# Kernel optimization log

Measured on AMD Instinct MI355X. Metric: run time of the kernel, lower is better.

Reference implementation:

```python
import jax, jax.numpy as jnp
import numpy as np

B, N, H = 8, 128, 512   # batch, num_sent (n == m required by the 'all' branch), hidden_size
D = 2 * H               # bi-LSTM output dim
SCALE = 0.05


def setup_inputs() -> dict:
    key = jax.random.key(0)
    ks = jax.random.split(key, 24)
    p = lambda k, shape: (jax.random.normal(k, shape, dtype=jnp.float32) * SCALE)
    return {
        "x0_enc": jax.random.normal(ks[0], (B, N, D), dtype=jnp.float32),
        "x1_enc": jax.random.normal(ks[1], (B, N, D), dtype=jnp.float32),
        # concat_attention
        "Wc1": p(ks[2], (D, H)), "Wc2": p(ks[3], (D, H)), "vc": p(ks[4], (H,)),
        # bilinear_attention
        "Wb": p(ks[5], (D, D)),
        # dot_attention x2 (separate params)
        "Wd1": p(ks[6], (D, H)), "vd1": p(ks[7], (H,)),
        "Wd2": p(ks[8], (D, H)), "vd2": p(ks[9], (H,)),
        # minus_attention (Ws/vs are unused in forward)
        "Wm": p(ks[10], (D, H)), "vm": p(ks[11], (H,)),
        # aggregation_layer
        "Wq": p(ks[12], (D, H)), "vq": p(ks[13], (H,)),
        "Wp1": p(ks[14], (2 * D, H)), "Wp2": p(ks[15], (D, H)), "vp": p(ks[16], (H,)),
        "Wpred": p(ks[17], (2 * D, 2)), "bpred": jnp.zeros((2,), dtype=jnp.float32),
    }


def _dot_att(x, y, Wd, vd):
    # sjt[b,m,n] = vd . tanh(Wd(x[b,n] * y[b,m]))  -- pairwise elementwise product + MLP
    z = jnp.tanh(jnp.einsum("bnd,bmd,dh->bmnh", x, y, Wd))  # [B,m,n,H]
    s = jnp.einsum("bmnh,h->bmn", z, vd)
    a = jax.nn.softmax(s, axis=2)
    return jnp.einsum("bmn,bnd->bmd", a, x)


def _minus_att(x, y, Wm, vm):
    # Wm is linear, so Wm(x_n - y_m) = (x@Wm)_n - (y@Wm)_m
    a, b = x @ Wm, y @ Wm                                    # [B,n,H], [B,m,H]
    z = jnp.tanh(a[:, None, :, :] - b[:, :, None, :])        # [B,m,n,H]
    s = jnp.einsum("bmnh,h->bmn", z, vm)
    att = jax.nn.softmax(s, axis=2)
    return jnp.einsum("bmn,bnd->bmd", att, x)


def _concat_att(x, y, Wc1, Wc2, vc):
    a, b = x @ Wc1, y @ Wc2                                  # [B,n,H], [B,m,H]
    z = jnp.tanh(a[:, None, :, :] + b[:, :, None, :])        # [B,m,n,H]
    s = jnp.einsum("bmnh,h->bmn", z, vc)
    att = jax.nn.softmax(s, axis=2)
    return jnp.einsum("bmn,bnd->bmd", att, x)


def _bilinear_att(x, y, Wb):
    s = jnp.einsum("bmd,bnd->bmn", y, x @ Wb)
    att = jax.nn.softmax(s, axis=2)
    return jnp.einsum("bmn,bnd->bmd", att, x)


def reference(x0_enc, x1_enc, Wc1, Wc2, vc, Wb, Wd1, vd1, Wd2, vd2, Wm, vm,
              Wq, vq, Wp1, Wp2, vp, Wpred, bpred):
    x0, x1 = x0_enc, x1_enc
    # attention_fx('all')
    qtc = _concat_att(x0, x1, Wc1, Wc2, vc)
    qtb = _bilinear_att(x0, x1, Wb)
    qts = _dot_att(x0, x1, Wd1, vd1)
    qtd = _dot_att(x1, x0, Wd2, vd2)
    qtm = _minus_att(x0, x1, Wm, vm)
    agg_res = jnp.max(jnp.stack([x1, qts, qtc, qtd, qtb, qtm], axis=0), axis=0)  # [B,m,2H]
    # MultiAtt: dropout is identity in eval
    agg_rep = jnp.concatenate([x1, agg_res], axis=2)                             # [B,m,4H]
    # aggregation_layer
    sj = jnp.einsum("bnh,h->bn", jnp.tanh(x0 @ Wq), vq)
    rq = jnp.einsum("bn,bnd->bd", jax.nn.softmax(sj, axis=1), x0)                # [B,2H]
    t = agg_rep @ Wp1 + (rq @ Wp2)[:, None, :]                                   # [B,m,H]
    sp = jax.nn.softmax(jnp.einsum("bmh,h->bm", t, vp), axis=1)
    rp = jnp.einsum("bm,bmd->bd", sp, agg_rep)                                   # [B,4H]
    out = jax.nn.relu(rp @ Wpred + bpred)                                        # [B,2]
    return out
```

## Files before the change

kernel.cpp:

```cpp
#include <hip/hip_runtime.h>
#include <hip/hip_bf16.h>

static constexpr int Bc = 8, Nc = 128, Dc = 1024, Hc = 512;
static constexpr int BM = Bc * Nc;

typedef _Float16 half8 __attribute__((ext_vector_type(8)));
typedef __fp16 fp16x2 __attribute__((ext_vector_type(2)));
typedef float floatx4 __attribute__((ext_vector_type(4)));

__device__ __forceinline__ float fast_tanh(float x) {
  x = fminf(fmaxf(x, -15.f), 15.f);
  float e = __expf(2.f * x);
  return (e - 1.f) / (e + 1.f);
}

__device__ __forceinline__ unsigned pkh2(float a, float b) {
  fp16x2 h = __builtin_amdgcn_cvt_pkrtz(a, b);
  return __builtin_bit_cast(unsigned, h);
}

__device__ __forceinline__ ushort f2h(float f) {
  _Float16 h = (_Float16)f;
  return __builtin_bit_cast(ushort, h);
}

__device__ __forceinline__ float block_sum256(float v, float* buf4) {
  #pragma unroll
  for (int o = 32; o; o >>= 1) v += __shfl_down(v, o, 64);
  const int w = threadIdx.x >> 6, lane = threadIdx.x & 63;
  if (lane == 0) buf4[w] = v;
  __syncthreads();
  return buf4[0] + buf4[1] + buf4[2] + buf4[3];
}

__global__ __launch_bounds__(256) void cvt_both(const float* __restrict__ x0,
                                                const float* __restrict__ x1,
                                                ushort* __restrict__ o0,
                                                ushort* __restrict__ o1) {
  int bi = blockIdx.x;
  const float* src = (bi < 512) ? x0 : x1;
  ushort* dst = (bi < 512) ? o0 : o1;
  int off = (bi & 511);
  int i = (off * 256 + threadIdx.x) * 8;
  float4 a = *reinterpret_cast<const float4*>(&src[i]);
  float4 b = *reinterpret_cast<const float4*>(&src[i + 4]);
  uint4 o;
  o.x = pkh2(a.x, a.y); o.y = pkh2(a.z, a.w);
  o.z = pkh2(b.x, b.y); o.w = pkh2(b.z, b.w);
  *reinterpret_cast<uint4*>(&dst[i]) = o;
}

struct TJobs {
  const float* src[7];
  ushort* dst[7];
  int J[7];
};
__global__ __launch_bounds__(256) void conv_transpose_multi(TJobs jobs) {
  const int job = blockIdx.z;
  const int J = jobs.J[job];
  const int h0 = blockIdx.y * 64;
  if (h0 >= J) return;
  const float* W = jobs.src[job];
  ushort* WT = jobs.dst[job];
  __shared__ float tile[64][65];
  const int d0 = blockIdx.x * 64;
  const int tid = threadIdx.x;
  #pragma unroll
  for (int i = 0; i < 16; i++) {
    int idx = tid + i * 256;
    int dd = idx >> 6, hh = idx & 63;
    tile[dd][hh] = W[(size_t)(d0 + dd) * J + h0 + hh];
  }
  __syncthreads();
  #pragma unroll
  for (int i = 0; i < 16; i++) {
    int idx = tid + i * 256;
    int hh = idx >> 6, dd = idx & 63;
    WT[(size_t)(h0 + hh) * Dc + d0 + dd] = f2h(tile[dd][hh]);
  }
}

__global__ __launch_bounds__(256) void gemm_bt(const ushort* __restrict__ A,
                                               const ushort* __restrict__ BT,
                                               float* __restrict__ Cf,
                                               ushort* __restrict__ Ch,
                                               int K, int ldc,
                                               size_t sA, size_t sB, size_t sC) {
  const int bz = blockIdx.z;
  A  += (size_t)bz * sA;
  BT += (size_t)bz * sB;
  const int m0 = blockIdx.y * 64, n0 = blockIdx.x * 64;
  __shared__ __align__(16) ushort Asl[64][40];
  __shared__ __align__(16) ushort Bsl[64][40];
  const int tid = threadIdx.x, wave = tid >> 6, lane = tid & 63;
  const int quad = lane >> 4, l15 = lane & 15;
  const int wr = (wave & 1) * 32, wc = (wave >> 1) * 32;
  const int rSt = tid >> 2, kSt8 = (tid & 3) * 8;
  floatx4 acc[2][2];
  #pragma unroll
  for (int i = 0; i < 2; i++)
    #pragma unroll
    for (int j = 0; j < 2; j++) acc[i][j] = (floatx4){0.f, 0.f, 0.f, 0.f};
  uint4 pa = *reinterpret_cast<const uint4*>(&A[(size_t)(m0 + rSt) * K + kSt8]);
  uint4 pb = *reinterpret_cast<const uint4*>(&BT[(size_t)(n0 + rSt) * K + kSt8]);
  for (int k0 = 0; k0 < K; k0 += 32) {
    *reinterpret_cast<uint4*>(&Asl[rSt][kSt8]) = pa;
    *reinterpret_cast<uint4*>(&Bsl[rSt][kSt8]) = pb;
    __syncthreads();
    if (k0 + 32 < K) {
      pa = *reinterpret_cast<const uint4*>(&A[(size_t)(m0 + rSt) * K + k0 + 32 + kSt8]);
      pb = *reinterpret_cast<const uint4*>(&BT[(size_t)(n0 + rSt) * K + k0 + 32 + kSt8]);
    }
    half8 af[2], bb[2];
    #pragma unroll
    for (int i = 0; i < 2; i++)
      af[i] = *reinterpret_cast<const half8*>(&Asl[wr + i * 16 + l15][quad * 8]);
    #pragma unroll
    for (int j = 0; j < 2; j++)
      bb[j] = *reinterpret_cast<const half8*>(&Bsl[wc + j * 16 + l15][quad * 8]);
    #pragma unroll
    for (int i = 0; i < 2; i++)
      #pragma unroll
      for (int j = 0; j < 2; j++)
        acc[i][j] = __builtin_amdgcn_mfma_f32_16x16x32_f16(af[i], bb[j], acc[i][j], 0, 0, 0);
    __syncthreads();
  }
  if (Ch) {
    #pragma unroll
    for (int i = 0; i < 2; i++)
      #pragma unroll
      for (int j = 0; j < 2; j++)
        #pragma unroll
        for (int r = 0; r < 4; r++) {
          int row = m0 + wr + i * 16 + quad * 4 + r;
          int col = n0 + wc + j * 16 + l15;
          Ch[(size_t)bz * sC + (size_t)row * ldc + col] = f2h(acc[i][j][r]);
        }
  } else {
    #pragma unroll
    for (int i = 0; i < 2; i++)
      #pragma unroll
      for (int j = 0; j < 2; j++)
        #pragma unroll
        for (int r = 0; r < 4; r++) {
          int row = m0 + wr + i * 16 + quad * 4 + r;
          int col = n0 + wc + j * 16 + l15;
          Cf[(size_t)bz * sC + (size_t)row * ldc + col] = acc[i][j][r];
        }
  }
}

__global__ __launch_bounds__(256, 2) void dot_scores_mfma4(const ushort* __restrict__ X0h,
                                                           const ushort* __restrict__ X1h,
                                                           const ushort* __restrict__ WdT1,
                                                           const ushort* __restrict__ WdT2,
                                                           const float* __restrict__ vd1,
                                                           const float* __restrict__ vd2,
                                                           float* __restrict__ Sd) {
  const int which = blockIdx.z;
  const ushort* Xh = which ? X1h : X0h;
  const ushort* Yh = which ? X0h : X1h;
  const ushort* WdT = which ? WdT2 : WdT1;
  const float* v = which ? vd2 : vd1;
  float* S = Sd + (size_t)which * (BM * Nc);

  const int bm = blockIdx.y;
  const int b = bm >> 7;
  const int hBase = blockIdx.x * 256;
  const int tid = threadIdx.x;
  const int wave = tid >> 6, lane = tid & 63;
  const int quad = lane >> 4, l15 = lane & 15;
  const int wn = wave & 1, wh = wave >> 1;

  __shared__ __align__(16) char smraw[65536];
  ushort (*As0)[40] = (ushort(*)[40])(smraw);
  ushort (*As1)[40] = (ushort(*)[40])(smraw + 10240);
  ushort (*Bs0)[40] = (ushort(*)[40])(smraw + 20480);
  ushort (*Bs1)[40] = (ushort(*)[40])(smraw + 40960);
  ushort* ylh = (ushort*)(smraw + 61440);
  float (*red)[33] = (float(*)[33])(smraw);

  {
    const uint* Yrow = (const uint*)(Yh + (size_t)bm * Dc);
    uint* dst = (uint*)ylh;
    for (int i = tid; i < Dc / 2; i += 256) dst[i] = Yrow[i];
  }

  floatx4 acc[4][8];
  #pragma unroll
  for (int i = 0; i < 4; i++)
    #pragma unroll
    for (int j = 0; j < 8; j++) acc[i][j] = (floatx4){0.f, 0.f, 0.f, 0.f};

  const ushort* Xb = Xh + (size_t)b * Nc * Dc;
  const int nSt = tid >> 2;
  const int kSt8 = (tid & 3) * 8;

  auto stage = [&](int k0, ushort (*Asb)[40], ushort (*Bsb)[40]) {
    half8 yv = *reinterpret_cast<const half8*>(&ylh[k0 + kSt8]);
    #pragma unroll
    for (int p = 0; p < 2; p++) {
      const int n = p * 64 + nSt;
      half8 xv = *reinterpret_cast<const half8*>(&Xb[(size_t)n * Dc + k0 + kSt8]);
      half8 prod = xv * yv;
      *reinterpret_cast<half8*>(&Asb[n][kSt8]) = prod;
    }
    #pragma unroll
    for (int r = 0; r < 4; r++)
      *reinterpret_cast<uint4*>(&Bsb[r * 64 + nSt][kSt8]) =
          *reinterpret_cast<const uint4*>(&WdT[(size_t)(hBase + r * 64 + nSt) * Dc + k0 + kSt8]);
  };

  auto mfma_step = [&](ushort (*Asb)[40], ushort (*Bsb)[40]) {
    half8 af[4], bfr[8];
    #pragma unroll
    for (int i = 0; i < 4; i++)
      af[i] = *reinterpret_cast<const half8*>(&Asb[wn * 64 + i * 16 + l15][quad * 8]);
    #pragma unroll
    for (int j = 0; j < 8; j++)
      bfr[j] = *reinterpret_cast<const half8*>(&Bsb[wh * 128 + j * 16 + l15][quad * 8]);
    #pragma unroll
    for (int i = 0; i < 4; i++)
      #pragma unroll
      for (int j = 0; j < 8; j++)
        acc[i][j] = __builtin_amdgcn_mfma_f32_16x16x32_f16(af[i], bfr[j], acc[i][j], 0, 0, 0);
  };

  __syncthreads();
  stage(0, As0, Bs0);
  __syncthreads();
  #pragma unroll 1
  for (int s = 0; s < 32; s += 2) {
    if (s + 1 < 32) stage((s + 1) * 32, As1, Bs1);
    mfma_step(As0, Bs0);
    __syncthreads();
    if (s + 2 < 32) stage((s + 2) * 32, As0, Bs0);
    mfma_step(As1, Bs1);
    __syncthreads();
  }

  float vv[8];
  #pragma unroll
  for (int j = 0; j < 8; j++) vv[j] = v[hBase + wh * 128 + j * 16 + l15];
  #pragma unroll
  for (int i = 0; i < 4; i++)
    #pragma unroll
    for (int r = 0; r < 4; r++) {
      float p = 0.f;
      #pragma unroll
      for (int j = 0; j < 8; j++) p = fmaf(vv[j], fast_tanh(acc[i][j][r]), p);
      red[wn * 64 + i * 16 + quad * 4 + r][wh * 16 + l15] = p;
    }
  __syncthreads();
  if (tid < 128) {
    float s = 0.f;
    #pragma unroll
    for (int c = 0; c < 32; c++) s += red[tid][c];
    atomicAdd(&S[(size_t)bm * Nc + tid], s);
  }
}

__global__ __launch_bounds__(256) void addtanh_tiled2(const float* __restrict__ C1,
                                                      const float* __restrict__ C2,
                                                      const float* __restrict__ vc,
                                                      const float* __restrict__ vm,
                                                      float* __restrict__ Sc,
                                                      float* __restrict__ Sm) {
  const int nt = blockIdx.x, mt = blockIdx.y;
  const int which = blockIdx.z >> 3, b = blockIdx.z & 7;
  const float* Arow = C1 + which * 512;
  const float* Brow = C2 + which * 512;
  const float* v = which ? vm : vc;
  const float sign = which ? -1.f : 1.f;
  float* S = which ? Sm : Sc;
  __shared__ __align__(16) float at[16][516];
  __shared__ __align__(16) float bt2[16][516];
  __shared__ __align__(16) float vl[512];
  const int tid = threadIdx.x;
  #pragma unroll
  for (int p = 0; p < 8; p++) {
    int idx = p * 256 + tid;
    int r = idx >> 7, c4 = (idx & 127) * 4;
    *reinterpret_cast<float4*>(&at[r][c4]) =
        *reinterpret_cast<const float4*>(&Arow[(size_t)(b * Nc + nt * 16 + r) * 1024 + c4]);
    *reinterpret_cast<float4*>(&bt2[r][c4]) =
        *reinterpret_cast<const float4*>(&Brow[(size_t)(b * Nc + mt * 16 + r) * 1024 + c4]);
  }
  if (tid < 128)
    *reinterpret_cast<float4*>(&vl[tid * 4]) = *reinterpret_cast<const float4*>(&v[tid * 4]);
  __syncthreads();
  const int m = tid >> 4, n = tid & 15;
  float acc = 0.f;
  #pragma unroll 4
  for (int c = 0; c < 512; c += 4) {
    float4 av = *reinterpret_cast<const float4*>(&at[n][c]);
    float4 bv = *reinterpret_cast<const float4*>(&bt2[m][c]);
    float4 vv = *reinterpret_cast<const float4*>(&vl[c]);
    acc = fmaf(vv.x, fast_tanh(fmaf(sign, bv.x, av.x)), acc);
    acc = fmaf(vv.y, fast_tanh(fmaf(sign, bv.y, av.y)), acc);
    acc = fmaf(vv.z, fast_tanh(fmaf(sign, bv.z, av.z)), acc);
    acc = fmaf(vv.w, fast_tanh(fmaf(sign, bv.w, av.w)), acc);
  }
  S[(size_t)(b * Nc + mt * 16 + m) * Nc + nt * 16 + n] = acc;
}

__global__ __launch_bounds__(128) void softmax128(float* __restrict__ S) {
  const int row = blockIdx.x;
  const int tid = threadIdx.x;
  float x = S[(size_t)row * 128 + tid];
  __shared__ float mbuf[2], sbuf[2];
  float mx = x;
  #pragma unroll
  for (int o = 32; o; o >>= 1) mx = fmaxf(mx, __shfl_down(mx, o, 64));
  if ((tid & 63) == 0) mbuf[tid >> 6] = mx;
  __syncthreads();
  mx = fmaxf(mbuf[0], mbuf[1]);
  float e = __expf(x - mx);
  float sm = e;
  #pragma unroll
  for (int o = 32; o; o >>= 1) sm += __shfl_down(sm, o, 64);
  if ((tid & 63) == 0) sbuf[tid >> 6] = sm;
  __syncthreads();
  sm = sbuf[0] + sbuf[1];
  S[(size_t)row * 128 + tid] = e / sm;
}

#define FMA4(acc, s, v)                  \
  acc.x = fmaf(s, v.x, acc.x);           \
  acc.y = fmaf(s, v.y, acc.y);           \
  acc.z = fmaf(s, v.z, acc.z);           \
  acc.w = fmaf(s, v.w, acc.w)

__global__ __launch_bounds__(256) void agg_max(const float* __restrict__ x0,
                                               const float* __restrict__ x1,
                                               const float* __restrict__ Sc,
                                               const float* __restrict__ Sb,
                                               const float* __restrict__ Sd1,
                                               const float* __restrict__ Sd2,
                                               const float* __restrict__ Sm,
                                               float* __restrict__ agg) {
  const int bm = blockIdx.x;
  const int b = bm >> 7;
  const int tid = threadIdx.x;
  __shared__ float w[5][128];
  if (tid < 128) {
    w[0][tid] = Sc[(size_t)bm * Nc + tid];
    w[1][tid] = Sb[(size_t)bm * Nc + tid];
    w[2][tid] = Sd1[(size_t)bm * Nc + tid];
    w[3][tid] = Sd2[(size_t)bm * Nc + tid];
    w[4][tid] = Sm[(size_t)bm * Nc + tid];
  }
  __syncthreads();
  const int d0 = tid * 4;
  float4 qc = {0, 0, 0, 0}, qb = {0, 0, 0, 0}, qs = {0, 0, 0, 0};
  float4 qd = {0, 0, 0, 0}, qm = {0, 0, 0, 0};
  const float* X0b = x0 + (size_t)b * Nc * Dc;
  const float* X1b = x1 + (size_t)b * Nc * Dc;
  for (int n = 0; n < Nc; n++) {
    float4 xv = *reinterpret_cast<const float4*>(&X0b[(size_t)n * Dc + d0]);
    float4 yv = *reinterpret_cast<const float4*>(&X1b[(size_t)n * Dc + d0]);
    float wc = w[0][n], wb = w[1][n], ws = w[2][n], wd = w[3][n], wm = w[4][n];
    FMA4(qc, wc, xv);
    FMA4(qb, wb, xv);
    FMA4(qs, ws, xv);
    FMA4(qd, wd, yv);
    FMA4(qm, wm, xv);
  }
  float4 x1v = *reinterpret_cast<const float4*>(&x1[(size_t)bm * Dc + d0]);
  float4 r;
  r.x = fmaxf(x1v.x, fmaxf(fmaxf(qs.x, qc.x), fmaxf(fmaxf(qd.x, qb.x), qm.x)));
  r.y = fmaxf(x1v.y, fmaxf(fmaxf(qs.y, qc.y), fmaxf(fmaxf(qd.y, qb.y), qm.y)));
  r.z = fmaxf(x1v.z, fmaxf(fmaxf(qs.z, qc.z), fmaxf(fmaxf(qd.z, qb.z), qm.z)));
  r.w = fmaxf(x1v.w, fmaxf(fmaxf(qs.w, qc.w), fmaxf(fmaxf(qd.w, qb.w), qm.w)));
  *reinterpret_cast<float4*>(&agg[(size_t)bm * Dc + d0]) = r;
}

__global__ __launch_bounds__(64) void compute_u(const float* __restrict__ Wp1,
                                                const float* __restrict__ vp,
                                                float* __restrict__ u) {
  const int d2 = blockIdx.x;
  const int tid = threadIdx.x;
  float p = 0.f;
  #pragma unroll
  for (int h = tid; h < Hc; h += 64) p = fmaf(Wp1[(size_t)d2 * Hc + h], vp[h], p);
  #pragma unroll
  for (int o = 32; o; o >>= 1) p += __shfl_down(p, o, 64);
  if (tid == 0) u[d2] = p;
}

__global__ __launch_bounds__(256) void final_scores(const float* __restrict__ x1,
                                                    const float* __restrict__ agg,
                                                    const float* __restrict__ u,
                                                    float* __restrict__ score) {
  const int bm = blockIdx.x;
  const int tid = threadIdx.x;
  float p = 0.f;
  #pragma unroll
  for (int d = tid; d < Dc; d += 256)
    p = fmaf(x1[(size_t)bm * Dc + d], u[d], fmaf(agg[(size_t)bm * Dc + d], u[Dc + d], p));
  __shared__ float buf4[4];
  p = block_sum256(p, buf4);
  if (tid == 0) score[bm] = p;
}

__global__ __launch_bounds__(256) void final_out(const float* __restrict__ x1,
                                                 const float* __restrict__ agg,
                                                 const float* __restrict__ score,
                                                 const float* __restrict__ Wpred,
                                                 const float* __restrict__ bpred,
                                                 float* __restrict__ out) {
  const int b = blockIdx.x;
  const int tid = threadIdx.x;
  __shared__ float spL[128];
  __shared__ float mbuf[2], sbuf[2];
  if (tid < 128) {
    float x = score[b * Nc + tid];
    float mx = x;
    #pragma unroll
    for (int o = 32; o; o >>= 1) mx = fmaxf(mx, __shfl_down(mx, o, 64));
    if ((tid & 63) == 0) mbuf[tid >> 6] = mx;
  }
  __syncthreads();
  if (tid < 128) {
    float x = score[b * Nc + tid];
    float mx = fmaxf(mbuf[0], mbuf[1]);
    float e = __expf(x - mx);
    float sm = e;
    #pragma unroll
    for (int o = 32; o; o >>= 1) sm += __shfl_down(sm, o, 64);
    if ((tid & 63) == 0) sbuf[tid >> 6] = sm;
    spL[tid] = e;
  }
  __syncthreads();
  const float inv = 1.f / (sbuf[0] + sbuf[1]);
  const int d2 = tid * 8;
  float w0[8], w1[8];
  #pragma unroll
  for (int i = 0; i < 8; i++) {
    w0[i] = Wpred[(size_t)(d2 + i) * 2 + 0];
    w1[i] = Wpred[(size_t)(d2 + i) * 2 + 1];
  }
  const float* src = (d2 < Dc) ? (x1 + (size_t)b * Nc * Dc + d2)
                               : (agg + (size_t)b * Nc * Dc + (d2 - Dc));
  float p0 = 0.f, p1 = 0.f;
  for (int m = 0; m < Nc; m++) {
    float s = spL[m] * inv;
    const float* r = src + (size_t)m * Dc;
    #pragma unroll
    for (int i = 0; i < 8; i++) {
      float sc = s * r[i];
      p0 = fmaf(sc, w0[i], p0);
      p1 = fmaf(sc, w1[i], p1);
    }
  }
  #pragma unroll
  for (int o = 32; o; o >>= 1) {
    p0 += __shfl_down(p0, o, 64);
    p1 += __shfl_down(p1, o, 64);
  }
  __shared__ float r0[4], r1[4];
  const int w = tid >> 6, lane = tid & 63;
  if (lane == 0) { r0[w] = p0; r1[w] = p1; }
  __syncthreads();
  if (tid == 0) {
    float q0 = r0[0] + r0[1] + r0[2] + r0[3] + bpred[0];
    float q1 = r1[0] + r1[1] + r1[2] + r1[3] + bpred[1];
    out[b * 2 + 0] = fmaxf(q0, 0.f);
    out[b * 2 + 1] = fmaxf(q1, 0.f);
  }
}

extern "C" void kernel_launch(void* const* d_in, const int* in_sizes, int n_in,
                              void* d_out, int out_size, void* d_ws, size_t ws_size,
                              hipStream_t stream) {
  const float* x0    = (const float*)d_in[0];
  const float* x1    = (const float*)d_in[1];
  const float* Wc1   = (const float*)d_in[2];
  const float* Wc2   = (const float*)d_in[3];
  const float* vc    = (const float*)d_in[4];
  const float* Wb    = (const float*)d_in[5];
  const float* Wd1   = (const float*)d_in[6];
  const float* vd1   = (const float*)d_in[7];
  const float* Wd2   = (const float*)d_in[8];
  const float* vd2   = (const float*)d_in[9];
  const float* Wm    = (const float*)d_in[10];
  const float* vm    = (const float*)d_in[11];
  const float* Wp1   = (const float*)d_in[14];
  const float* vp    = (const float*)d_in[16];
  const float* Wpred = (const float*)d_in[17];
  const float* bpred = (const float*)d_in[18];
  float* out = (float*)d_out;

  float* ws = (float*)d_ws;
  float* C1     = ws;
  float* C2     = C1 + 1048576;
  float* sc     = C2 + 1048576;
  float* sb     = sc + 131072;
  float* sd1    = sb + 131072;
  float* sd2    = sd1 + 131072;
  float* smv    = sd2 + 131072;
  float* u      = smv + 131072;
  float* score2 = u + 2048;
  ushort* x0h   = (ushort*)(score2 + 1024);
  ushort* x1h   = x0h + 1048576;
  ushort* W1T   = x1h + 1048576;
  ushort* W2T   = W1T + 1048576;
  ushort* WbT   = W2T + 1048576;
  ushort* xWbh  = WbT + 1048576;
  ushort* wdT1  = xWbh + 1048576;
  ushort* wdT2  = wdT1 + 524288;
  float* agg    = C1;

  cvt_both<<<1024, 256, 0, stream>>>(x0, x1, x0h, x1h);
  TJobs tj;
  tj.src[0] = Wd1; tj.dst[0] = wdT1;            tj.J[0] = Hc;
  tj.src[1] = Wd2; tj.dst[1] = wdT2;            tj.J[1] = Hc;
  tj.src[2] = Wc1; tj.dst[2] = W1T;             tj.J[2] = Hc;
  tj.src[3] = Wm;  tj.dst[3] = W1T + 512 * Dc;  tj.J[3] = Hc;
  tj.src[4] = Wc2; tj.dst[4] = W2T;             tj.J[4] = Hc;
  tj.src[5] = Wm;  tj.dst[5] = W2T + 512 * Dc;  tj.J[5] = Hc;
  tj.src[6] = Wb;  tj.dst[6] = WbT;             tj.J[6] = Dc;
  conv_transpose_multi<<<dim3(16, 16, 7), 256, 0, stream>>>(tj);

  gemm_bt<<<dim3(16, 16, 1), 256, 0, stream>>>(x0h, W1T, C1, nullptr, Dc, 1024, 0, 0, 0);
  gemm_bt<<<dim3(16, 16, 1), 256, 0, stream>>>(x1h, W2T, C2, nullptr, Dc, 1024, 0, 0, 0);
  gemm_bt<<<dim3(16, 16, 1), 256, 0, stream>>>(x0h, WbT, nullptr, xWbh, Dc, 1024, 0, 0, 0);
  gemm_bt<<<dim3(2, 2, 8), 256, 0, stream>>>(x1h, xWbh, sb, nullptr, Dc, 128,
                                             131072, 131072, 16384);

  addtanh_tiled2<<<dim3(8, 8, 16), 256, 0, stream>>>(C1, C2, vc, vm, sc, smv);

  (void)hipMemsetAsync(sd1, 0, 2 * 131072 * sizeof(float), stream);
  dot_scores_mfma4<<<dim3(2, BM, 2), 256, 0, stream>>>(x0h, x1h, wdT1, wdT2, vd1, vd2, sd1);

  softmax128<<<5 * BM, 128, 0, stream>>>(sc);

  agg_max<<<BM, 256, 0, stream>>>(x0, x1, sc, sb, sd1, sd2, smv, agg);

  compute_u<<<2 * Dc, 64, 0, stream>>>(Wp1, vp, u);
  final_scores<<<BM, 256, 0, stream>>>(x1, agg, u, score2);
  final_out<<<Bc, 256, 0, stream>>>(x1, agg, score2, Wpred, bpred, out);
}
```

Measured before the change: 651.0 us.

## Pre-swizzle Wd into k-chunked layout, load dot-score A operands directly, fuse final scores

The Wd weights are now written by the transpose kernel in a k-chunked, XOR-swizzled layout, so the dot-score kernel can copy B tiles into LDS with plain contiguous stores and read them without bank conflicts. The A operand (x*y product) no longer goes through LDS: each lane loads its MFMA fragment straight from global memory and multiplies it by y in registers. This cuts LDS footprint and traffic, which may allow more occupancy. The final_scores kernel is folded into agg_max, and compute_u is moved earlier in the launch order. The trade-off is uncoalesced per-lane global loads for A and more register pressure from the prefetch buffers.

```diff
diff --git a/kernel.cpp b/kernel.cpp
--- a/kernel.cpp
+++ b/kernel.cpp
@@ -54,6 +54,7 @@
   const float* src[7];
   ushort* dst[7];
   int J[7];
+  int swz[7];
 };
 __global__ __launch_bounds__(256) void conv_transpose_multi(TJobs jobs) {
   const int job = blockIdx.z;
@@ -62,6 +63,7 @@
   if (h0 >= J) return;
   const float* W = jobs.src[job];
   ushort* WT = jobs.dst[job];
+  const int swz = jobs.swz[job];
   __shared__ float tile[64][65];
   const int d0 = blockIdx.x * 64;
   const int tid = threadIdx.x;
@@ -76,7 +78,14 @@
   for (int i = 0; i < 16; i++) {
     int idx = tid + i * 256;
     int hh = idx >> 6, dd = idx & 63;
-    WT[(size_t)(h0 + hh) * Dc + d0 + dd] = f2h(tile[dd][hh]);
+    size_t oidx;
+    if (swz) {
+      oidx = (size_t)((d0 + dd) >> 5) * (512 * 32) + (size_t)(h0 + hh) * 32 +
+             ((((dd >> 3) & 3) ^ ((hh >> 1) & 3)) * 8) + (dd & 7);
+    } else {
+      oidx = (size_t)(h0 + hh) * Dc + (d0 + dd);
+    }
+    WT[oidx] = f2h(tile[dd][hh]);
   }
 }
 
@@ -150,17 +159,17 @@
   }
 }
 
-__global__ __launch_bounds__(256, 2) void dot_scores_mfma4(const ushort* __restrict__ X0h,
+__global__ __launch_bounds__(256, 2) void dot_scores_mfma5(const ushort* __restrict__ X0h,
                                                            const ushort* __restrict__ X1h,
-                                                           const ushort* __restrict__ WdT1,
-                                                           const ushort* __restrict__ WdT2,
+                                                           const ushort* __restrict__ WdS1,
+                                                           const ushort* __restrict__ WdS2,
                                                            const float* __restrict__ vd1,
                                                            const float* __restrict__ vd2,
                                                            float* __restrict__ Sd) {
   const int which = blockIdx.z;
   const ushort* Xh = which ? X1h : X0h;
   const ushort* Yh = which ? X0h : X1h;
-  const ushort* WdT = which ? WdT2 : WdT1;
+  const ushort* WdS = which ? WdS2 : WdS1;
   const float* v = which ? vd2 : vd1;
   float* S = Sd + (size_t)which * (BM * Nc);
 
@@ -172,18 +181,17 @@
   const int quad = lane >> 4, l15 = lane & 15;
   const int wn = wave & 1, wh = wave >> 1;
 
-  __shared__ __align__(16) char smraw[65536];
-  ushort (*As0)[40] = (ushort(*)[40])(smraw);
-  ushort (*As1)[40] = (ushort(*)[40])(smraw + 10240);
-  ushort (*Bs0)[40] = (ushort(*)[40])(smraw + 20480);
-  ushort (*Bs1)[40] = (ushort(*)[40])(smraw + 40960);
-  ushort* ylh = (ushort*)(smraw + 61440);
+  __shared__ __align__(16) char smraw[16384 * 2 + 2048];
+  ushort* Bs0 = (ushort*)(smraw);
+  ushort* Bs1 = (ushort*)(smraw + 16384);
+  ushort* ylh = (ushort*)(smraw + 32768);
   float (*red)[33] = (float(*)[33])(smraw);
 
   {
     const uint* Yrow = (const uint*)(Yh + (size_t)bm * Dc);
     uint* dst = (uint*)ylh;
-    for (int i = tid; i < Dc / 2; i += 256) dst[i] = Yrow[i];
+    #pragma unroll
+    for (int i = 0; i < 2; i++) dst[tid + i * 256] = Yrow[tid + i * 256];
   }
 
   floatx4 acc[4][8];
@@ -193,49 +201,73 @@
     for (int j = 0; j < 8; j++) acc[i][j] = (floatx4){0.f, 0.f, 0.f, 0.f};
 
   const ushort* Xb = Xh + (size_t)b * Nc * Dc;
-  const int nSt = tid >> 2;
-  const int kSt8 = (tid & 3) * 8;
-
-  auto stage = [&](int k0, ushort (*Asb)[40], ushort (*Bsb)[40]) {
-    half8 yv = *reinterpret_cast<const half8*>(&ylh[k0 + kSt8]);
-    #pragma unroll
-    for (int p = 0; p < 2; p++) {
-      const int n = p * 64 + nSt;
-      half8 xv = *reinterpret_cast<const half8*>(&Xb[(size_t)n * Dc + k0 + kSt8]);
-      half8 prod = xv * yv;
-      *reinterpret_cast<half8*>(&Asb[n][kSt8]) = prod;
-    }
-    #pragma unroll
-    for (int r = 0; r < 4; r++)
-      *reinterpret_cast<uint4*>(&Bsb[r * 64 + nSt][kSt8]) =
-          *reinterpret_cast<const uint4*>(&WdT[(size_t)(hBase + r * 64 + nSt) * Dc + k0 + kSt8]);
+  int xoff[4];
+  #pragma unroll
+  for (int i = 0; i < 4; i++) xoff[i] = (wn * 64 + i * 16 + l15) * Dc + quad * 8;
+  const ushort* wsrc = WdS + hBase * 32 + tid * 8;
+  const int bswz = (quad ^ ((l15 >> 1) & 3)) * 8;
+  const int brow = (wh * 128 + l15) * 32;
+
+  half8 xv[4], prod[4];
+  uint4 pa[4];
+
+  auto loadA = [&](int s) {
+    #pragma unroll
+    for (int i = 0; i < 4; i++)
+      xv[i] = *reinterpret_cast<const half8*>(Xb + xoff[i] + s * 32);
   };
-
-  auto mfma_step = [&](ushort (*Asb)[40], ushort (*Bsb)[40]) {
-    half8 af[4], bfr[8];
+  auto loadB = [&](int s) {
+    const ushort* g = wsrc + s * 16384;
     #pragma unroll
     for (int i = 0; i < 4; i++)
-      af[i] = *reinterpret_cast<const half8*>(&Asb[wn * 64 + i * 16 + l15][quad * 8]);
+      pa[i] = *reinterpret_cast<const uint4*>(g + i * 2048);
+  };
+  auto writeB = [&](ushort* Bsb) {
+    #pragma unroll
+    for (int i = 0; i < 4; i++)
+      *reinterpret_cast<uint4*>(Bsb + tid * 8 + i * 2048) = pa[i];
+  };
+  auto mulA = [&](int s) {
+    half8 yv = *reinterpret_cast<const half8*>(&ylh[s * 32 + quad * 8]);
+    #pragma unroll
+    for (int i = 0; i < 4; i++) prod[i] = xv[i] * yv;
+  };
+  auto mfma_step = [&](const ushort* Bsb) {
+    half8 bfr[8];
     #pragma unroll
     for (int j = 0; j < 8; j++)
-      bfr[j] = *reinterpret_cast<const half8*>(&Bsb[wh * 128 + j * 16 + l15][quad * 8]);
+      bfr[j] = *reinterpret_cast<const half8*>(Bsb + brow + j * 512 + bswz);
     #pragma unroll
     for (int i = 0; i < 4; i++)
       #pragma unroll
       for (int j = 0; j < 8; j++)
-        acc[i][j] = __builtin_amdgcn_mfma_f32_16x16x32_f16(af[i], bfr[j], acc[i][j], 0, 0, 0);
+        acc[i][j] = __builtin_amdgcn_mfma_f32_16x16x32_f16(prod[i], bfr[j], acc[i][j], 0, 0, 0);
   };
 
   __syncthreads();
-  stage(0, As0, Bs0);
-  __syncthreads();
+  loadA(0);
+  loadB(0);
+  writeB(Bs0);
+  mulA(0);
+  __syncthreads();
+
   #pragma unroll 1
   for (int s = 0; s < 32; s += 2) {
-    if (s + 1 < 32) stage((s + 1) * 32, As1, Bs1);
-    mfma_step(As0, Bs0);
+    loadA(s + 1);
+    loadB(s + 1);
+    mfma_step(Bs0);
+    writeB(Bs1);
+    mulA(s + 1);
     __syncthreads();
-    if (s + 2 < 32) stage((s + 2) * 32, As0, Bs0);
-    mfma_step(As1, Bs1);
+    if (s + 2 < 32) {
+      loadA(s + 2);
+      loadB(s + 2);
+    }
+    mfma_step(Bs1);
+    if (s + 2 < 32) {
+      writeB(Bs0);
+      mulA(s + 2);
+    }
     __syncthreads();
   }
 
@@ -338,7 +370,9 @@
                                                const float* __restrict__ Sd1,
                                                const float* __restrict__ Sd2,
                                                const float* __restrict__ Sm,
-                                               float* __restrict__ agg) {
+                                               const float* __restrict__ u,
+                                               float* __restrict__ agg,
+                                               float* __restrict__ score) {
   const int bm = blockIdx.x;
   const int b = bm >> 7;
   const int tid = threadIdx.x;
@@ -373,6 +407,13 @@
   r.z = fmaxf(x1v.z, fmaxf(fmaxf(qs.z, qc.z), fmaxf(fmaxf(qd.z, qb.z), qm.z)));
   r.w = fmaxf(x1v.w, fmaxf(fmaxf(qs.w, qc.w), fmaxf(fmaxf(qd.w, qb.w), qm.w)));
   *reinterpret_cast<float4*>(&agg[(size_t)bm * Dc + d0]) = r;
+  float4 u1 = *reinterpret_cast<const float4*>(&u[d0]);
+  float4 u2 = *reinterpret_cast<const float4*>(&u[Dc + d0]);
+  float p = x1v.x * u1.x + x1v.y * u1.y + x1v.z * u1.z + x1v.w * u1.w +
+            r.x * u2.x + r.y * u2.y + r.z * u2.z + r.w * u2.w;
+  __shared__ float buf4[4];
+  p = block_sum256(p, buf4);
+  if (tid == 0) score[bm] = p;
 }
 
 __global__ __launch_bounds__(64) void compute_u(const float* __restrict__ Wp1,
@@ -386,21 +427,6 @@
   #pragma unroll
   for (int o = 32; o; o >>= 1) p += __shfl_down(p, o, 64);
   if (tid == 0) u[d2] = p;
-}
-
-__global__ __launch_bounds__(256) void final_scores(const float* __restrict__ x1,
-                                                    const float* __restrict__ agg,
-                                                    const float* __restrict__ u,
-                                                    float* __restrict__ score) {
-  const int bm = blockIdx.x;
-  const int tid = threadIdx.x;
-  float p = 0.f;
-  #pragma unroll
-  for (int d = tid; d < Dc; d += 256)
-    p = fmaf(x1[(size_t)bm * Dc + d], u[d], fmaf(agg[(size_t)bm * Dc + d], u[Dc + d], p));
-  __shared__ float buf4[4];
-  p = block_sum256(p, buf4);
-  if (tid == 0) score[bm] = p;
 }
 
 __global__ __launch_bounds__(256) void final_out(const float* __restrict__ x1,
@@ -507,20 +533,21 @@
   ushort* W2T   = W1T + 1048576;
   ushort* WbT   = W2T + 1048576;
   ushort* xWbh  = WbT + 1048576;
-  ushort* wdT1  = xWbh + 1048576;
-  ushort* wdT2  = wdT1 + 524288;
+  ushort* wdS1  = xWbh + 1048576;
+  ushort* wdS2  = wdS1 + 524288;
   float* agg    = C1;
 
   cvt_both<<<1024, 256, 0, stream>>>(x0, x1, x0h, x1h);
   TJobs tj;
-  tj.src[0] = Wd1; tj.dst[0] = wdT1;            tj.J[0] = Hc;
-  tj.src[1] = Wd2; tj.dst[1] = wdT2;            tj.J[1] = Hc;
-  tj.src[2] = Wc1; tj.dst[2] = W1T;             tj.J[2] = Hc;
-  tj.src[3] = Wm;  tj.dst[3] = W1T + 512 * Dc;  tj.J[3] = Hc;
-  tj.src[4] = Wc2; tj.dst[4] = W2T;             tj.J[4] = Hc;
-  tj.src[5] = Wm;  tj.dst[5] = W2T + 512 * Dc;  tj.J[5] = Hc;
-  tj.src[6] = Wb;  tj.dst[6] = WbT;             tj.J[6] = Dc;
+  tj.src[0] = Wd1; tj.dst[0] = wdS1;            tj.J[0] = Hc; tj.swz[0] = 1;
+  tj.src[1] = Wd2; tj.dst[1] = wdS2;            tj.J[1] = Hc; tj.swz[1] = 1;
+  tj.src[2] = Wc1; tj.dst[2] = W1T;             tj.J[2] = Hc; tj.swz[2] = 0;
+  tj.src[3] = Wm;  tj.dst[3] = W1T + 512 * Dc;  tj.J[3] = Hc; tj.swz[3] = 0;
+  tj.src[4] = Wc2; tj.dst[4] = W2T;             tj.J[4] = Hc; tj.swz[4] = 0;
+  tj.src[5] = Wm;  tj.dst[5] = W2T + 512 * Dc;  tj.J[5] = Hc; tj.swz[5] = 0;
+  tj.src[6] = Wb;  tj.dst[6] = WbT;             tj.J[6] = Dc; tj.swz[6] = 0;
   conv_transpose_multi<<<dim3(16, 16, 7), 256, 0, stream>>>(tj);
+  compute_u<<<2 * Dc, 64, 0, stream>>>(Wp1, vp, u);
 
   gemm_bt<<<dim3(16, 16, 1), 256, 0, stream>>>(x0h, W1T, C1, nullptr, Dc, 1024, 0, 0, 0);
   gemm_bt<<<dim3(16, 16, 1), 256, 0, stream>>>(x1h, W2T, C2, nullptr, Dc, 1024, 0, 0, 0);
@@ -531,13 +558,11 @@
   addtanh_tiled2<<<dim3(8, 8, 16), 256, 0, stream>>>(C1, C2, vc, vm, sc, smv);
 
   (void)hipMemsetAsync(sd1, 0, 2 * 131072 * sizeof(float), stream);
-  dot_scores_mfma4<<<dim3(2, BM, 2), 256, 0, stream>>>(x0h, x1h, wdT1, wdT2, vd1, vd2, sd1);
+  dot_scores_mfma5<<<dim3(2, BM, 2), 256, 0, stream>>>(x0h, x1h, wdS1, wdS2, vd1, vd2, sd1);
 
   softmax128<<<5 * BM, 128, 0, stream>>>(sc);
 
-  agg_max<<<BM, 256, 0, stream>>>(x0, x1, sc, sb, sd1, sd2, smv, agg);
-
-  compute_u<<<2 * Dc, 64, 0, stream>>>(Wp1, vp, u);
-  final_scores<<<BM, 256, 0, stream>>>(x1, agg, u, score2);
+  agg_max<<<BM, 256, 0, stream>>>(x0, x1, sc, sb, sd1, sd2, smv, u, agg, score2);
+
   final_out<<<Bc, 256, 0, stream>>>(x1, agg, score2, Wpred, bpred, out);
 }
```

After: 898.9 us. 38.1% more time.
